# Optimization experiments

Hardware: AMD Instinct MI355X
Metric: run time of the kernel (lower is better)

Reference implementation:

```python
import jax, jax.numpy as jnp
import numpy as np

ALPHA = 0.2  # LeakyReLU negative slope
NEG = -9e15


def gat_layer(h, adj, W, a):
    # Faithful to the torch GAT: e_ij = leakyrelu(a^T [Wh_i || Wh_j])
    # = leakyrelu(a_src . Wh_i + a_dst . Wh_j); avoids the NxNx2F materialization.
    Wh = h @ W                              # [N, F]
    Fo = W.shape[1]
    a_src, a_dst = a[:Fo, 0], a[Fo:, 0]
    e = jax.nn.leaky_relu(
        (Wh @ a_src)[:, None] + (Wh @ a_dst)[None, :], negative_slope=ALPHA
    )                                        # [N, N]
    e = jnp.where(adj > 0, e, NEG)
    att = jax.nn.softmax(e, axis=1)          # dropout p=0 (eval)
    return jax.nn.elu(att @ Wh)


def gru_cell(x, h, W_ih, W_hh, b_ih, b_hh):
    # PyTorch GRUCell semantics.
    gi = x @ W_ih.T + b_ih                   # [N, 3F]
    gh = h @ W_hh.T + b_hh
    i_r, i_z, i_n = jnp.split(gi, 3, axis=1)
    h_r, h_z, h_n = jnp.split(gh, 3, axis=1)
    r = jax.nn.sigmoid(i_r + h_r)
    z = jax.nn.sigmoid(i_z + h_z)
    n = jnp.tanh(i_n + r * h_n)
    return (1.0 - z) * n + z * h


def setup_inputs() -> dict:
    key = jax.random.key(0)
    ks = jax.random.split(key, 10)
    N, nfeat, nhid, nout = 8192, 256, 128, 128
    x = jax.random.normal(ks[0], (N, nfeat), dtype=jnp.float32)
    # sparse random binary adjacency (~32 avg degree) + self loops
    adj = (jax.random.uniform(ks[1], (N, N)) < 0.004).astype(jnp.float32)
    adj = jnp.maximum(adj, jnp.eye(N, dtype=jnp.float32))
    h_prev = jnp.zeros((N, nout), dtype=jnp.float32)

    def xavier(k, shape, gain=1.414):
        fan_in, fan_out = shape[0], shape[1]
        b = gain * np.sqrt(6.0 / (fan_in + fan_out))
        return jax.random.uniform(k, shape, jnp.float32, -b, b)

    W1 = xavier(ks[2], (nfeat, nhid))
    a1 = xavier(ks[3], (2 * nhid, 1))
    W2 = xavier(ks[4], (nhid, nout))
    a2 = xavier(ks[5], (2 * nout, 1))
    s = 1.0 / np.sqrt(nout)
    W_ih = jax.random.uniform(ks[6], (3 * nout, nout), jnp.float32, -s, s)
    W_hh = jax.random.uniform(ks[7], (3 * nout, nout), jnp.float32, -s, s)
    b_ih = jax.random.uniform(ks[8], (3 * nout,), jnp.float32, -s, s)
    b_hh = jax.random.uniform(ks[9], (3 * nout,), jnp.float32, -s, s)
    return {"x": x, "adj": adj, "h_prev": h_prev, "W1": W1, "a1": a1,
            "W2": W2, "a2": a2, "W_ih": W_ih, "W_hh": W_hh,
            "b_ih": b_ih, "b_hh": b_hh}


def reference(x, adj, h_prev, W1, a1, W2, a2, W_ih, W_hh, b_ih, b_hh):
    x1 = gat_layer(x, adj, W1, a1)
    h_spat = gat_layer(x1, adj, W2, a2)
    return gru_cell(h_spat, h_prev, W_ih, W_hh, b_ih, b_hh)
```

## Files before the change

### kernel.cpp

```cpp
#include <hip/hip_runtime.h>
#include <math.h>

#define N_NODES 8192
#define CAP 128
#define LRELU_ALPHA 0.2f

typedef float v4f __attribute__((ext_vector_type(4)));

template <int K>
__device__ __forceinline__ void gemm_from_lds(
    int r0, int t, const float* As, const float* __restrict__ W,
    const float* __restrict__ a, float* __restrict__ Wh, float* __restrict__ src,
    float* __restrict__ dst, float (*red)[4][2]) {
  int c = t & 127, half = t >> 7;
  float acc[4] = {0.f, 0.f, 0.f, 0.f};
  const float* Asl = As + (half * 4) * K;
#pragma unroll 2
  for (int k = 0; k < K; k += 4) {
    float w0 = W[(k + 0) * 128 + c];
    float w1 = W[(k + 1) * 128 + c];
    float w2 = W[(k + 2) * 128 + c];
    float w3 = W[(k + 3) * 128 + c];
#pragma unroll
    for (int r = 0; r < 4; r++) {
      float4 av = *(const float4*)&Asl[r * K + k];
      acc[r] += av.x * w0 + av.y * w1 + av.z * w2 + av.w * w3;
    }
  }
  float as = a[c], ad = a[128 + c];
  int wv_id = t >> 6, lane = t & 63;
#pragma unroll
  for (int r = 0; r < 4; r++) {
    int row = half * 4 + r;
    Wh[(size_t)(r0 + row) * 128 + c] = acc[r];
    float s = acc[r] * as, d = acc[r] * ad;
#pragma unroll
    for (int off = 32; off; off >>= 1) {
      s += __shfl_xor(s, off);
      d += __shfl_xor(d, off);
    }
    if (lane == 0) { red[wv_id][r][0] = s; red[wv_id][r][1] = d; }
  }
  __syncthreads();
  if (t < 8) {
    int wa = (t < 4) ? 0 : 2, rr = t & 3;
    src[r0 + t] = red[wa][rr][0] + red[wa + 1][rr][0];
    dst[r0 + t] = red[wa][rr][1] + red[wa + 1][rr][1];
  }
}

__device__ __forceinline__ float2 agg_node_wave(
    int i, int lane, const float* __restrict__ Wh, const float* __restrict__ src,
    const float* __restrict__ dst, const int* __restrict__ idxbuf,
    const int* __restrict__ counts) {
  int c = counts[i];
  float si = src[i];
  int j0 = 0, j1 = 0;
  float e0 = -1e30f, e1 = -1e30f;
  if (lane < c) {
    j0 = idxbuf[(size_t)i * CAP + lane];
    float xv = si + dst[j0];
    e0 = xv > 0.f ? xv : LRELU_ALPHA * xv;
  }
  if (lane + 64 < c) {
    j1 = idxbuf[(size_t)i * CAP + lane + 64];
    float xv = si + dst[j1];
    e1 = xv > 0.f ? xv : LRELU_ALPHA * xv;
  }
  float m = fmaxf(e0, e1);
#pragma unroll
  for (int off = 32; off; off >>= 1) m = fmaxf(m, __shfl_xor(m, off));
  float w0 = (lane < c) ? expf(e0 - m) : 0.f;
  float w1 = (lane + 64 < c) ? expf(e1 - m) : 0.f;
  float s = w0 + w1;
#pragma unroll
  for (int off = 32; off; off >>= 1) s += __shfl_xor(s, off);
  float inv = 1.f / s;
  const float2* Wh2 = (const float2*)Wh;
  float ax = 0.f, ay = 0.f;
  int cc = c < 64 ? c : 64;
  for (int k = 0; k < cc; k += 8) {
    float w_[8]; int j_[8]; float2 v_[8];
#pragma unroll
    for (int q = 0; q < 8; q++) { w_[q] = __shfl(w0, k + q); j_[q] = __shfl(j0, k + q); }
#pragma unroll
    for (int q = 0; q < 8; q++) v_[q] = Wh2[(size_t)j_[q] * 64 + lane];
#pragma unroll
    for (int q = 0; q < 8; q++) { ax += w_[q] * v_[q].x; ay += w_[q] * v_[q].y; }
  }
  if (c > 64) {
    for (int k = 64; k < c; k++) {
      float wk = __shfl(w1, k - 64);
      int jk = __shfl(j1, k - 64);
      float2 v = Wh2[(size_t)jk * 64 + lane];
      ax += wk * v.x; ay += wk * v.y;
    }
  }
  ax *= inv; ay *= inv;
  return make_float2(ax > 0.f ? ax : expf(ax) - 1.f,
                     ay > 0.f ? ay : expf(ay) - 1.f);
}

__device__ __forceinline__ void gru_tile(
    int i0, int t, const float* tile, const float* hs, const float* __restrict__ WiT,
    const float* __restrict__ WhT, const float* __restrict__ b_ih,
    const float* __restrict__ b_hh, float* __restrict__ outp) {
  int c = t & 127, half = t >> 7;
  const float* xsl = tile + half * 4 * 128;
  const float* hsl = hs + half * 4 * 128;
  float ai[3][4] = {{0.f}}, ah[3][4] = {{0.f}};
  for (int k = 0; k < 128; k += 4) {
    float4 xv[4], hv[4];
#pragma unroll
    for (int r = 0; r < 4; r++) {
      xv[r] = *(const float4*)&xsl[r * 128 + k];
      hv[r] = *(const float4*)&hsl[r * 128 + k];
    }
#pragma unroll
    for (int g = 0; g < 3; g++) {
      int base = g * 128 + c;
      float wi0 = WiT[(k + 0) * 384 + base], wi1 = WiT[(k + 1) * 384 + base];
      float wi2 = WiT[(k + 2) * 384 + base], wi3 = WiT[(k + 3) * 384 + base];
      float wh0 = WhT[(k + 0) * 384 + base], wh1 = WhT[(k + 1) * 384 + base];
      float wh2 = WhT[(k + 2) * 384 + base], wh3 = WhT[(k + 3) * 384 + base];
#pragma unroll
      for (int r = 0; r < 4; r++) {
        ai[g][r] += xv[r].x * wi0 + xv[r].y * wi1 + xv[r].z * wi2 + xv[r].w * wi3;
        ah[g][r] += hv[r].x * wh0 + hv[r].y * wh1 + hv[r].z * wh2 + hv[r].w * wh3;
      }
    }
  }
  float bi0 = b_ih[c], bi1 = b_ih[128 + c], bi2 = b_ih[256 + c];
  float bh0 = b_hh[c], bh1 = b_hh[128 + c], bh2 = b_hh[256 + c];
#pragma unroll
  for (int r = 0; r < 4; r++) {
    float rg = 1.f / (1.f + expf(-(ai[0][r] + bi0 + ah[0][r] + bh0)));
    float zg = 1.f / (1.f + expf(-(ai[1][r] + bi1 + ah[1][r] + bh1)));
    float n = tanhf(ai[2][r] + bi2 + rg * (ah[2][r] + bh2));
    outp[(size_t)(i0 + half * 4 + r) * 128 + c] =
        (1.f - zg) * n + zg * hsl[r * 128 + c];
  }
}

__global__ __launch_bounds__(256) void kA(
    const float* __restrict__ adj, int* __restrict__ idxbuf, int* __restrict__ counts,
    const float* __restrict__ x, const float* __restrict__ W1, const float* __restrict__ a1,
    float* __restrict__ Wh1, float* __restrict__ src1, float* __restrict__ dst1,
    const float* __restrict__ Wi, const float* __restrict__ Whm, float* __restrict__ WiT,
    float* __restrict__ WhT) {
  __shared__ float As[8 * 256];
  __shared__ float red[4][4][2];
  __shared__ int jn[CAP];
  __shared__ int cnt;
  int t = threadIdx.x, b = blockIdx.x;
  if (b < 1024) {
    const float4* Ab4 = (const float4*)(x + (size_t)b * 8 * 256);
    float4* As4 = (float4*)As;
#pragma unroll
    for (int l = t; l < 8 * 256 / 4; l += 256) As4[l] = Ab4[l];
    __syncthreads();
    gemm_from_lds<256>(b * 8, t, As, W1, a1, Wh1, src1, dst1, red);
  } else if (b < 1088) {
    for (int n = (b - 1024) * 256 + t; n < 384 * 128; n += 64 * 256) {
      int r = n >> 7, c = n & 127;
      WiT[c * 384 + r] = Wi[n];
      WhT[c * 384 + r] = Whm[n];
    }
  } else {
    int row = b - 1088;
    if (t == 0) cnt = 0;
    __syncthreads();
    const v4f* rowp = (const v4f*)(adj + (size_t)row * N_NODES);
    v4f v[8];
#pragma unroll
    for (int u = 0; u < 8; u++) v[u] = __builtin_nontemporal_load(rowp + t + 256 * u);
#pragma unroll
    for (int u = 0; u < 8; u++) {
      int n = (v[u].x > 0.f) + (v[u].y > 0.f) + (v[u].z > 0.f) + (v[u].w > 0.f);
      if (n) {
        int p = atomicAdd(&cnt, n);
        int j0 = (t + 256 * u) * 4;
        if (v[u].x > 0.f) { if (p < CAP) jn[p] = j0;     p++; }
        if (v[u].y > 0.f) { if (p < CAP) jn[p] = j0 + 1; p++; }
        if (v[u].z > 0.f) { if (p < CAP) jn[p] = j0 + 2; p++; }
        if (v[u].w > 0.f) { if (p < CAP) jn[p] = j0 + 3; p++; }
      }
    }
    __syncthreads();
    int c = cnt > CAP ? CAP : cnt;
    if (t < c) idxbuf[(size_t)row * CAP + t] = jn[t];
    if (t == 0) counts[row] = c;
  }
}

__global__ __launch_bounds__(256) void kB(
    const float* __restrict__ Wh1, const float* __restrict__ src1,
    const float* __restrict__ dst1, const int* __restrict__ idxbuf,
    const int* __restrict__ counts, const float* __restrict__ W2, const float* __restrict__ a2,
    float* __restrict__ Wh2, float* __restrict__ src2, float* __restrict__ dst2) {
  __shared__ float tile[8 * 128];
  __shared__ float red[4][4][2];
  int t = threadIdx.x, b = blockIdx.x;
  int i0 = b * 8;
  int wv = t >> 6, lane = t & 63;
  float2 r0 = agg_node_wave(i0 + wv, lane, Wh1, src1, dst1, idxbuf, counts);
  *(float2*)&tile[wv * 128 + 2 * lane] = r0;
  float2 r1 = agg_node_wave(i0 + 4 + wv, lane, Wh1, src1, dst1, idxbuf, counts);
  *(float2*)&tile[(4 + wv) * 128 + 2 * lane] = r1;
  __syncthreads();
  gemm_from_lds<128>(i0, t, tile, W2, a2, Wh2, src2, dst2, red);
}

__global__ __launch_bounds__(256) void kC(
    const float* __restrict__ Wh2, const float* __restrict__ src2,
    const float* __restrict__ dst2, const int* __restrict__ idxbuf,
    const int* __restrict__ counts, const float* __restrict__ hprev,
    const float* __restrict__ WiT, const float* __restrict__ WhT,
    const float* __restrict__ b_ih, const float* __restrict__ b_hh, float* __restrict__ outp) {
  __shared__ float tile[8 * 128];
  __shared__ float hs[8 * 128];
  int t = threadIdx.x, b = blockIdx.x;
  int i0 = b * 8;
  ((float4*)hs)[t] = ((const float4*)(hprev + (size_t)i0 * 128))[t];
  int wv = t >> 6, lane = t & 63;
  float2 r0 = agg_node_wave(i0 + wv, lane, Wh2, src2, dst2, idxbuf, counts);
  *(float2*)&tile[wv * 128 + 2 * lane] = r0;
  float2 r1 = agg_node_wave(i0 + 4 + wv, lane, Wh2, src2, dst2, idxbuf, counts);
  *(float2*)&tile[(4 + wv) * 128 + 2 * lane] = r1;
  __syncthreads();
  gru_tile(i0, t, tile, hs, WiT, WhT, b_ih, b_hh, outp);
}

extern "C" void kernel_launch(void* const* d_in, const int* in_sizes, int n_in,
                              void* d_out, int out_size, void* d_ws, size_t ws_size,
                              hipStream_t stream) {
  const float* x     = (const float*)d_in[0];
  const float* adj   = (const float*)d_in[1];
  const float* hprev = (const float*)d_in[2];
  const float* W1    = (const float*)d_in[3];
  const float* a1    = (const float*)d_in[4];
  const float* W2    = (const float*)d_in[5];
  const float* a2    = (const float*)d_in[6];
  const float* Wi    = (const float*)d_in[7];
  const float* Whm   = (const float*)d_in[8];
  const float* b_ih  = (const float*)d_in[9];
  const float* b_hh  = (const float*)d_in[10];
  float* outp = (float*)d_out;

  char* p = (char*)d_ws;
  float* Wh1    = (float*)p; p += (size_t)N_NODES * 128 * 4;
  float* Wh2    = (float*)p; p += (size_t)N_NODES * 128 * 4;
  float* src1   = (float*)p; p += (size_t)N_NODES * 4;
  float* dst1   = (float*)p; p += (size_t)N_NODES * 4;
  float* src2   = (float*)p; p += (size_t)N_NODES * 4;
  float* dst2   = (float*)p; p += (size_t)N_NODES * 4;
  float* WiT    = (float*)p; p += (size_t)384 * 128 * 4;
  float* WhT    = (float*)p; p += (size_t)384 * 128 * 4;
  int*   counts = (int*)p;   p += (size_t)N_NODES * 4;
  int*   idxbuf = (int*)p;   p += (size_t)N_NODES * CAP * 4;

  kA<<<1024 + 64 + N_NODES, 256, 0, stream>>>(adj, idxbuf, counts, x, W1, a1, Wh1, src1, dst1,
                                              Wi, Whm, WiT, WhT);
  kB<<<N_NODES / 8, 256, 0, stream>>>(Wh1, src1, dst1, idxbuf, counts, W2, a2, Wh2, src2, dst2);
  kC<<<N_NODES / 8, 256, 0, stream>>>(Wh2, src2, dst2, idxbuf, counts, hprev, WiT, WhT, b_ih,
                                      b_hh, outp);
}
```

Baseline: 432.2 us.

## Use 512-thread blocks with one node per wave and LDS-staged neighbor weights

The aggregation kernels kB and kC now launch 512 threads per block, so each of the 8 waves handles one node instead of 4 waves handling two nodes each. The GEMM and GRU tiles are rewritten to split the 8 rows over 4 row groups of 2. The neighbor weight/index pairs are staged in LDS and read back as float4, replacing the per-neighbor shuffle broadcasts. The aim is more concurrent gather latency hiding and fewer shuffle instructions, at the cost of more threads per block and extra LDS traffic.

```diff
diff --git a/kernel.cpp b/kernel.cpp
--- a/kernel.cpp
+++ b/kernel.cpp
@@ -49,10 +49,51 @@
   }
 }
 
+__device__ __forceinline__ void gemm8_512(
+    int r0, int t, const float* As, const float* __restrict__ W,
+    const float* __restrict__ a, float* __restrict__ Wh, float* __restrict__ src,
+    float* __restrict__ dst, float (*red)[2][2]) {
+  int c = t & 127, g = t >> 7;
+  float acc[2] = {0.f, 0.f};
+  const float* Asl = As + (g * 2) * 128;
+#pragma unroll 4
+  for (int k = 0; k < 128; k += 4) {
+    float w0 = W[(k + 0) * 128 + c];
+    float w1 = W[(k + 1) * 128 + c];
+    float w2 = W[(k + 2) * 128 + c];
+    float w3 = W[(k + 3) * 128 + c];
+#pragma unroll
+    for (int r = 0; r < 2; r++) {
+      float4 av = *(const float4*)&Asl[r * 128 + k];
+      acc[r] += av.x * w0 + av.y * w1 + av.z * w2 + av.w * w3;
+    }
+  }
+  float as = a[c], ad = a[128 + c];
+  int wv = t >> 6, lane = t & 63;
+#pragma unroll
+  for (int r = 0; r < 2; r++) {
+    int row = g * 2 + r;
+    Wh[(size_t)(r0 + row) * 128 + c] = acc[r];
+    float s = acc[r] * as, d = acc[r] * ad;
+#pragma unroll
+    for (int off = 32; off; off >>= 1) {
+      s += __shfl_xor(s, off);
+      d += __shfl_xor(d, off);
+    }
+    if (lane == 0) { red[wv][r][0] = s; red[wv][r][1] = d; }
+  }
+  __syncthreads();
+  if (t < 8) {
+    int g2 = t >> 1, rr = t & 1;
+    src[r0 + t] = red[2 * g2][rr][0] + red[2 * g2 + 1][rr][0];
+    dst[r0 + t] = red[2 * g2][rr][1] + red[2 * g2 + 1][rr][1];
+  }
+}
+
 __device__ __forceinline__ float2 agg_node_wave(
     int i, int lane, const float* __restrict__ Wh, const float* __restrict__ src,
     const float* __restrict__ dst, const int* __restrict__ idxbuf,
-    const int* __restrict__ counts) {
+    const int* __restrict__ counts, float2* jw) {
   int c = counts[i];
   float si = src[i];
   int j0 = 0, j1 = 0;
@@ -76,17 +117,27 @@
 #pragma unroll
   for (int off = 32; off; off >>= 1) s += __shfl_xor(s, off);
   float inv = 1.f / s;
+  jw[lane] = make_float2(w0, __int_as_float(j0));
   const float2* Wh2 = (const float2*)Wh;
   float ax = 0.f, ay = 0.f;
   int cc = c < 64 ? c : 64;
   for (int k = 0; k < cc; k += 8) {
-    float w_[8]; int j_[8]; float2 v_[8];
-#pragma unroll
-    for (int q = 0; q < 8; q++) { w_[q] = __shfl(w0, k + q); j_[q] = __shfl(j0, k + q); }
-#pragma unroll
-    for (int q = 0; q < 8; q++) v_[q] = Wh2[(size_t)j_[q] * 64 + lane];
-#pragma unroll
-    for (int q = 0; q < 8; q++) { ax += w_[q] * v_[q].x; ay += w_[q] * v_[q].y; }
+    float4 p0 = *(const float4*)&jw[k];
+    float4 p1 = *(const float4*)&jw[k + 2];
+    float4 p2 = *(const float4*)&jw[k + 4];
+    float4 p3 = *(const float4*)&jw[k + 6];
+    float2 v0 = Wh2[(size_t)(unsigned)__float_as_int(p0.y) * 64 + lane];
+    float2 v1 = Wh2[(size_t)(unsigned)__float_as_int(p0.w) * 64 + lane];
+    float2 v2 = Wh2[(size_t)(unsigned)__float_as_int(p1.y) * 64 + lane];
+    float2 v3 = Wh2[(size_t)(unsigned)__float_as_int(p1.w) * 64 + lane];
+    float2 v4 = Wh2[(size_t)(unsigned)__float_as_int(p2.y) * 64 + lane];
+    float2 v5 = Wh2[(size_t)(unsigned)__float_as_int(p2.w) * 64 + lane];
+    float2 v6 = Wh2[(size_t)(unsigned)__float_as_int(p3.y) * 64 + lane];
+    float2 v7 = Wh2[(size_t)(unsigned)__float_as_int(p3.w) * 64 + lane];
+    ax += p0.x * v0.x + p0.z * v1.x + p1.x * v2.x + p1.z * v3.x +
+          p2.x * v4.x + p2.z * v5.x + p3.x * v6.x + p3.z * v7.x;
+    ay += p0.x * v0.y + p0.z * v1.y + p1.x * v2.y + p1.z * v3.y +
+          p2.x * v4.y + p2.z * v5.y + p3.x * v6.y + p3.z * v7.y;
   }
   if (c > 64) {
     for (int k = 64; k < c; k++) {
@@ -101,43 +152,43 @@
                      ay > 0.f ? ay : expf(ay) - 1.f);
 }
 
-__device__ __forceinline__ void gru_tile(
+__device__ __forceinline__ void gru_512(
     int i0, int t, const float* tile, const float* hs, const float* __restrict__ WiT,
     const float* __restrict__ WhT, const float* __restrict__ b_ih,
     const float* __restrict__ b_hh, float* __restrict__ outp) {
-  int c = t & 127, half = t >> 7;
-  const float* xsl = tile + half * 4 * 128;
-  const float* hsl = hs + half * 4 * 128;
-  float ai[3][4] = {{0.f}}, ah[3][4] = {{0.f}};
+  int c = t & 127, g = t >> 7;
+  const float* xsl = tile + g * 2 * 128;
+  const float* hsl = hs + g * 2 * 128;
+  float ai[3][2] = {{0.f}}, ah[3][2] = {{0.f}};
   for (int k = 0; k < 128; k += 4) {
-    float4 xv[4], hv[4];
-#pragma unroll
-    for (int r = 0; r < 4; r++) {
+    float4 xv[2], hv[2];
+#pragma unroll
+    for (int r = 0; r < 2; r++) {
       xv[r] = *(const float4*)&xsl[r * 128 + k];
       hv[r] = *(const float4*)&hsl[r * 128 + k];
     }
 #pragma unroll
-    for (int g = 0; g < 3; g++) {
-      int base = g * 128 + c;
+    for (int q = 0; q < 3; q++) {
+      int base = q * 128 + c;
       float wi0 = WiT[(k + 0) * 384 + base], wi1 = WiT[(k + 1) * 384 + base];
       float wi2 = WiT[(k + 2) * 384 + base], wi3 = WiT[(k + 3) * 384 + base];
       float wh0 = WhT[(k + 0) * 384 + base], wh1 = WhT[(k + 1) * 384 + base];
       float wh2 = WhT[(k + 2) * 384 + base], wh3 = WhT[(k + 3) * 384 + base];
 #pragma unroll
-      for (int r = 0; r < 4; r++) {
-        ai[g][r] += xv[r].x * wi0 + xv[r].y * wi1 + xv[r].z * wi2 + xv[r].w * wi3;
-        ah[g][r] += hv[r].x * wh0 + hv[r].y * wh1 + hv[r].z * wh2 + hv[r].w * wh3;
+      for (int r = 0; r < 2; r++) {
+        ai[q][r] += xv[r].x * wi0 + xv[r].y * wi1 + xv[r].z * wi2 + xv[r].w * wi3;
+        ah[q][r] += hv[r].x * wh0 + hv[r].y * wh1 + hv[r].z * wh2 + hv[r].w * wh3;
       }
     }
   }
   float bi0 = b_ih[c], bi1 = b_ih[128 + c], bi2 = b_ih[256 + c];
   float bh0 = b_hh[c], bh1 = b_hh[128 + c], bh2 = b_hh[256 + c];
 #pragma unroll
-  for (int r = 0; r < 4; r++) {
+  for (int r = 0; r < 2; r++) {
     float rg = 1.f / (1.f + expf(-(ai[0][r] + bi0 + ah[0][r] + bh0)));
     float zg = 1.f / (1.f + expf(-(ai[1][r] + bi1 + ah[1][r] + bh1)));
     float n = tanhf(ai[2][r] + bi2 + rg * (ah[2][r] + bh2));
-    outp[(size_t)(i0 + half * 4 + r) * 128 + c] =
+    outp[(size_t)(i0 + g * 2 + r) * 128 + c] =
         (1.f - zg) * n + zg * hsl[r * 128 + c];
   }
 }
@@ -193,25 +244,24 @@
   }
 }
 
-__global__ __launch_bounds__(256) void kB(
+__global__ __launch_bounds__(512, 8) void kB(
     const float* __restrict__ Wh1, const float* __restrict__ src1,
     const float* __restrict__ dst1, const int* __restrict__ idxbuf,
     const int* __restrict__ counts, const float* __restrict__ W2, const float* __restrict__ a2,
     float* __restrict__ Wh2, float* __restrict__ src2, float* __restrict__ dst2) {
   __shared__ float tile[8 * 128];
-  __shared__ float red[4][4][2];
+  __shared__ float red[8][2][2];
+  __shared__ float2 jwb[8][64];
   int t = threadIdx.x, b = blockIdx.x;
   int i0 = b * 8;
   int wv = t >> 6, lane = t & 63;
-  float2 r0 = agg_node_wave(i0 + wv, lane, Wh1, src1, dst1, idxbuf, counts);
+  float2 r0 = agg_node_wave(i0 + wv, lane, Wh1, src1, dst1, idxbuf, counts, jwb[wv]);
   *(float2*)&tile[wv * 128 + 2 * lane] = r0;
-  float2 r1 = agg_node_wave(i0 + 4 + wv, lane, Wh1, src1, dst1, idxbuf, counts);
-  *(float2*)&tile[(4 + wv) * 128 + 2 * lane] = r1;
   __syncthreads();
-  gemm_from_lds<128>(i0, t, tile, W2, a2, Wh2, src2, dst2, red);
-}
-
-__global__ __launch_bounds__(256) void kC(
+  gemm8_512(i0, t, tile, W2, a2, Wh2, src2, dst2, red);
+}
+
+__global__ __launch_bounds__(512, 8) void kC(
     const float* __restrict__ Wh2, const float* __restrict__ src2,
     const float* __restrict__ dst2, const int* __restrict__ idxbuf,
     const int* __restrict__ counts, const float* __restrict__ hprev,
@@ -219,16 +269,15 @@
     const float* __restrict__ b_ih, const float* __restrict__ b_hh, float* __restrict__ outp) {
   __shared__ float tile[8 * 128];
   __shared__ float hs[8 * 128];
+  __shared__ float2 jwb[8][64];
   int t = threadIdx.x, b = blockIdx.x;
   int i0 = b * 8;
-  ((float4*)hs)[t] = ((const float4*)(hprev + (size_t)i0 * 128))[t];
+  ((float2*)hs)[t] = ((const float2*)(hprev + (size_t)i0 * 128))[t];
   int wv = t >> 6, lane = t & 63;
-  float2 r0 = agg_node_wave(i0 + wv, lane, Wh2, src2, dst2, idxbuf, counts);
+  float2 r0 = agg_node_wave(i0 + wv, lane, Wh2, src2, dst2, idxbuf, counts, jwb[wv]);
   *(float2*)&tile[wv * 128 + 2 * lane] = r0;
-  float2 r1 = agg_node_wave(i0 + 4 + wv, lane, Wh2, src2, dst2, idxbuf, counts);
-  *(float2*)&tile[(4 + wv) * 128 + 2 * lane] = r1;
   __syncthreads();
-  gru_tile(i0, t, tile, hs, WiT, WhT, b_ih, b_hh, outp);
+  gru_512(i0, t, tile, hs, WiT, WhT, b_ih, b_hh, outp);
 }
 
 extern "C" void kernel_launch(void* const* d_in, const int* in_sizes, int n_in,
@@ -261,7 +310,7 @@
 
   kA<<<1024 + 64 + N_NODES, 256, 0, stream>>>(adj, idxbuf, counts, x, W1, a1, Wh1, src1, dst1,
                                               Wi, Whm, WiT, WhT);
-  kB<<<N_NODES / 8, 256, 0, stream>>>(Wh1, src1, dst1, idxbuf, counts, W2, a2, Wh2, src2, dst2);
-  kC<<<N_NODES / 8, 256, 0, stream>>>(Wh2, src2, dst2, idxbuf, counts, hprev, WiT, WhT, b_ih,
+  kB<<<N_NODES / 8, 512, 0, stream>>>(Wh1, src1, dst1, idxbuf, counts, W2, a2, Wh2, src2, dst2);
+  kC<<<N_NODES / 8, 512, 0, stream>>>(Wh2, src2, dst2, idxbuf, counts, hprev, WiT, WhT, b_ih,
                                       b_hh, outp);
 }
```

Result: slower. 447.9 us (+3.6%).
